# Performance work log

Hardware: AMD Instinct MI355X
Metric: run time of the kernel (lower is better)

Reference implementation:

```python
import jax, jax.numpy as jnp
import numpy as np

LEAKY = 0.2  # tf.nn.leaky_relu default alpha
E_SZ = [64, 64, 16]
F_SZ = [128, 128, 8]
N_MAPS, C, H, W = 64, 1, 32, 32
B = 8192


def _leaky(x):
    return jnp.where(x >= 0, x, LEAKY * x)


def func_theta(x, theta, sz, in_sz):
    # x: [B, in_sz]; theta: [B, total]; per-sample MLP with weights sliced from theta
    y = x
    offset = 0
    n = len(sz)
    for i, out_sz in enumerate(sz):
        w_sz = in_sz * out_sz
        Wm = theta[:, offset:offset + w_sz].reshape(-1, in_sz, out_sz)
        offset += w_sz
        b = theta[:, offset:offset + out_sz]
        offset += out_sz
        y = jnp.einsum('bi,bio->bo', y, Wm) + b
        if i < n - 1:
            y = _leaky(y)
        in_sz = out_sz
    return y


def setup_inputs() -> dict:
    key = jax.random.key(0)
    ks = jax.random.split(key, 16)

    def g(k, shape, scale):
        return (jax.random.normal(k, shape, dtype=jnp.float32) * scale)

    inp = {
        'indices': jax.random.randint(ks[0], (B,), 0, N_MAPS, dtype=jnp.int32),
        'states': jax.random.normal(ks[1], (B, 4), dtype=jnp.float32),
        'maps': jax.random.normal(ks[2], (N_MAPS, C, H, W), dtype=jnp.float32),
        'fc1_w': g(ks[3], (C * H * W, 256), 1.0 / np.sqrt(C * H * W)),
        'fc1_b': jnp.zeros((256,), jnp.float32),
        'fc2_w': g(ks[4], (256, 128), 1.0 / np.sqrt(256)),
        'fc2_b': jnp.zeros((128,), jnp.float32),
        'fc3_w': g(ks[5], (128, 128), 1.0 / np.sqrt(128)),
        'fc3_b': jnp.zeros((128,), jnp.float32),
        'bn_w': g(ks[6], (128, 32), 1.0 / np.sqrt(128)),
        'bn_b': jnp.zeros((32,), jnp.float32),
        'e_w': g(ks[7], (32, 5456), 1e-5),
        'e_b': g(ks[8], (5456,), 1e-3),
        'f_w': g(ks[9], (32, 21768), 1e-5),
        'f_b': g(ks[10], (21768,), 1e-3),
    }
    return inp


def reference(indices, states, maps, fc1_w, fc1_b, fc2_w, fc2_b, fc3_w, fc3_b,
              bn_w, bn_b, e_w, e_b, f_w, f_b):
    # gather maps per sample and flatten (NCHW -> NHWC transpose is a no-op after flatten
    # mathematically, but keep the exact data layout of the original)
    m = jnp.transpose(maps[indices], (0, 2, 3, 1)).astype(jnp.float32)  # [B,H,W,C]
    z = m.reshape(m.shape[0], -1)

    # hypernet trunk
    z = _leaky(z @ fc1_w + fc1_b)
    z = _leaky(z @ fc2_w + fc2_b)
    z = _leaky(z @ fc3_w + fc3_b)
    z = z @ bn_w + bn_b  # bottleneck, no activation
    theta_e = z @ e_w + e_b  # [B, 5456]
    theta_f = z @ f_w + f_b  # [B, 21768]

    S = states[:, 0:2]
    G = states[:, 2:4]
    e_s = func_theta(S, theta_e, E_SZ, 2)
    e_g = func_theta(G, theta_e, E_SZ, 2)
    zf = jnp.concatenate([e_s, e_g], axis=-1)  # [B, 32]
    ang = func_theta(zf, theta_f, F_SZ, 2 * E_SZ[-1])  # [B, 8]
    pts = jnp.concatenate([jnp.sin(ang), jnp.cos(ang)], axis=-1)  # [B, 16]
    return pts
```

## Files before the change

### kernel.cpp

```cpp
#include <hip/hip_runtime.h>
#include <hip/hip_bf16.h>


#define LEAKY 0.2f
#define NCLS 64
#define B_TOT 8192
#define NSLICE 4


__device__ __forceinline__ float lrelu(float x) { return x >= 0.f ? x : LEAKY * x; }

__global__ __launch_bounds__(1024) void backbone_bucket_kernel(
    const float* __restrict__ maps,
    const float* __restrict__ fc1_w, const float* __restrict__ fc1_b,
    const float* __restrict__ fc2_w, const float* __restrict__ fc2_b,
    const float* __restrict__ fc3_w, const float* __restrict__ fc3_b,
    const float* __restrict__ bn_w,  const float* __restrict__ bn_b,
    float* __restrict__ z,
    const int* __restrict__ idx, int* __restrict__ counts,
    int* __restrict__ offsets, int* __restrict__ perm)
{
    __shared__ float m[1024];
    __shared__ float red[1024];
    __shared__ float h1[256];
    __shared__ float h2[128];
    __shared__ float h3[128];
    __shared__ int cnt[16][64];
    __shared__ int wcur[16][64];

    const int t = threadIdx.x;

    if (blockIdx.x == 64) {
        const int w = t >> 6;
        cnt[w][t & 63] = 0;
        __syncthreads();
        int my[8];
#pragma unroll
        for (int r = 0; r < 8; ++r) {
            my[r] = idx[r * 1024 + t];
            atomicAdd(&cnt[w][my[r]], 1);
        }
        __syncthreads();
        if (t < 64) {
            int run = 0;
#pragma unroll
            for (int w2 = 0; w2 < 16; ++w2) {
                const int v = cnt[w2][t];
                wcur[w2][t] = run;
                run += v;
            }
            counts[t] = run;
            int x = run;
            for (int d = 1; d < 64; d <<= 1) {
                const int y = __shfl_up(x, d, 64);
                if (t >= d) x += y;
            }
            const int basec = x - run;
            offsets[t] = basec;
#pragma unroll
            for (int w2 = 0; w2 < 16; ++w2) wcur[w2][t] += basec;
        }
        __syncthreads();
#pragma unroll
        for (int r = 0; r < 8; ++r) {
            const int p = atomicAdd(&wcur[w][my[r]], 1);
            perm[p] = r * 1024 + t;
        }
        return;
    }

    const int c = blockIdx.x;
    m[t] = maps[(size_t)c * 1024 + t];
    __syncthreads();

    {
        const int o = t & 255, ks = t >> 8;
        const float* wp = fc1_w + o;
        float acc = 0.f;
#pragma unroll 8
        for (int i = 0; i < 256; ++i) {
            const int k = ks * 256 + i;
            acc += m[k] * wp[(size_t)k * 256];
        }
        red[t] = acc;
    }
    __syncthreads();
    if (t < 256)
        h1[t] = lrelu(fc1_b[t] + red[t] + red[256 + t] + red[512 + t] + red[768 + t]);
    __syncthreads();
    {
        const int o = t & 127, ks = t >> 7;
        float acc = 0.f;
#pragma unroll
        for (int i = 0; i < 32; ++i) {
            const int k = ks * 32 + i;
            acc += h1[k] * fc2_w[k * 128 + o];
        }
        red[t] = acc;
    }
    __syncthreads();
    if (t < 128) {
        float a = fc2_b[t];
#pragma unroll
        for (int r = 0; r < 8; ++r) a += red[r * 128 + t];
        h2[t] = lrelu(a);
    }
    __syncthreads();
    {
        const int o = t & 127, ks = t >> 7;
        float acc = 0.f;
#pragma unroll
        for (int i = 0; i < 16; ++i) {
            const int k = ks * 16 + i;
            acc += h2[k] * fc3_w[k * 128 + o];
        }
        red[t] = acc;
    }
    __syncthreads();
    if (t < 128) {
        float a = fc3_b[t];
#pragma unroll
        for (int r = 0; r < 8; ++r) a += red[r * 128 + t];
        h3[t] = lrelu(a);
    }
    __syncthreads();
    {
        const int o = t & 31, ks = t >> 5;
        float acc = 0.f;
#pragma unroll
        for (int i = 0; i < 4; ++i) {
            const int k = ks * 4 + i;
            acc += h3[k] * bn_w[k * 32 + o];
        }
        red[t] = acc;
    }
    __syncthreads();
    if (t < 32) {
        float a = bn_b[t];
#pragma unroll
        for (int r = 0; r < 32; ++r) a += red[r * 32 + t];
        z[c * 32 + t] = a;
    }
}

__global__ __launch_bounds__(256) void theta_kernel(
    const float* __restrict__ z,
    const float* __restrict__ e_w, const float* __restrict__ e_b,
    const float* __restrict__ f_w, const float* __restrict__ f_b,
    float* __restrict__ th_e, float* __restrict__ th_f)
{
    __shared__ __align__(16) float zl[2048];
    const int t = threadIdx.x;
    ((float4*)zl)[t]       = ((const float4*)z)[t];
    ((float4*)zl)[t + 256] = ((const float4*)z)[t + 256];
    __syncthreads();

    int j = blockIdx.x * 256 + t;
    const int cbase = blockIdx.y * 8;
    const float* wbase;
    float* op;
    int stride;
    float bias;
    if (j < 5456) {
        wbase = e_w + j; bias = e_b[j]; op = th_e + j; stride = 5456;
    } else {
        const int jj = j - 5456;
        if (jj >= 21768) return;
        wbase = f_w + jj; bias = f_b[jj]; op = th_f + jj; stride = 21768;
    }
    float wk[32];
#pragma unroll
    for (int k = 0; k < 32; ++k) wk[k] = wbase[(size_t)k * stride];

#pragma unroll
    for (int cc = 0; cc < 8; cc += 4) {
        const int c0 = cbase + cc;
        float a0 = bias, a1 = bias, a2 = bias, a3 = bias;
#pragma unroll
        for (int k4 = 0; k4 < 8; ++k4) {
            const float4 z0 = *(const float4*)&zl[(c0 + 0) * 32 + k4 * 4];
            const float4 z1 = *(const float4*)&zl[(c0 + 1) * 32 + k4 * 4];
            const float4 z2 = *(const float4*)&zl[(c0 + 2) * 32 + k4 * 4];
            const float4 z3 = *(const float4*)&zl[(c0 + 3) * 32 + k4 * 4];
            const float w0 = wk[k4 * 4], w1 = wk[k4 * 4 + 1];
            const float w2 = wk[k4 * 4 + 2], w3 = wk[k4 * 4 + 3];
            a0 += z0.x * w0 + z0.y * w1 + z0.z * w2 + z0.w * w3;
            a1 += z1.x * w0 + z1.y * w1 + z1.z * w2 + z1.w * w3;
            a2 += z2.x * w0 + z2.y * w1 + z2.z * w2 + z2.w * w3;
            a3 += z3.x * w0 + z3.y * w1 + z3.z * w2 + z3.w * w3;
        }
        op[(size_t)(c0 + 0) * stride] = a0;
        op[(size_t)(c0 + 1) * stride] = a1;
        op[(size_t)(c0 + 2) * stride] = a2;
        op[(size_t)(c0 + 3) * stride] = a3;
    }
}

#define ESTRIDE 68
#define FSTRIDE 132

__global__ __launch_bounds__(512) void func_kernel(
    const float* __restrict__ states,
    const float* __restrict__ th_e_all, const float* __restrict__ th_f_all,
    const int* __restrict__ counts, const int* __restrict__ offsets,
    const int* __restrict__ perm, float* __restrict__ out)
{
    __shared__ __align__(16) float wbuf[5392];
    __shared__ __align__(16) float w3fb[1160];
    __shared__ __align__(16) float actA[4352];
    __shared__ __align__(16) float actB[4352];

    const int c = blockIdx.x;
    const int s = blockIdx.y;
    const int nb   = counts[c];
    const int base = offsets[c];
    const int chunk = (nb + NSLICE - 1) / NSLICE;
    const int k0 = s * chunk;
    const int k1 = (nb < k0 + chunk) ? nb : (k0 + chunk);
    const int cnt = (k1 > k0) ? (k1 - k0) : 0;
    if (cnt == 0) return;

    const float* te = th_e_all + (size_t)c * 5456;
    const float* tf = th_f_all + (size_t)c * 21768;

    const int t  = threadIdx.x;
    const int b  = t & 31;
    const int ve = (t >> 5) & 1;
    const int vb = t & 63;
    const int ge = t >> 6;
    const int gf = t >> 5;
    const int cole = ge * 8;
    const int colf = gf * 8;
    const int eoff = vb * ESTRIDE;
    const int foff = b * FSTRIDE;

    for (int j = t * 4; j < 1160; j += 2048)
        *(float4*)&w3fb[j] = *(const float4*)&tf[20608 + j];
    for (int j = t * 4; j < 5392; j += 2048)
        *(float4*)&wbuf[j] = *(const float4*)&te[j];

    const int passes = (cnt + 31) >> 5;
    for (int p = 0; p < passes; ++p) {
        __syncthreads();
        if (p) {
            for (int j = t * 4; j < 5392; j += 2048)
                *(float4*)&wbuf[j] = *(const float4*)&te[j];
            __syncthreads();
        }

        const int kk = k0 + p * 32 + b;
        const bool valid = kk < k1;
        const int bi = valid ? perm[base + kk] : 0;
        const float2 sv = *(const float2*)&states[(size_t)bi * 4 + 2 * ve];

        {
            const float4 wa0 = *(const float4*)&wbuf[cole];
            const float4 wa1 = *(const float4*)&wbuf[cole + 4];
            const float4 wb0 = *(const float4*)&wbuf[64 + cole];
            const float4 wb1 = *(const float4*)&wbuf[64 + cole + 4];
            const float4 bb0 = *(const float4*)&wbuf[128 + cole];
            const float4 bb1 = *(const float4*)&wbuf[128 + cole + 4];
            float4 o0, o1;
            o0.x = lrelu(sv.x * wa0.x + sv.y * wb0.x + bb0.x);
            o0.y = lrelu(sv.x * wa0.y + sv.y * wb0.y + bb0.y);
            o0.z = lrelu(sv.x * wa0.z + sv.y * wb0.z + bb0.z);
            o0.w = lrelu(sv.x * wa0.w + sv.y * wb0.w + bb0.w);
            o1.x = lrelu(sv.x * wa1.x + sv.y * wb1.x + bb1.x);
            o1.y = lrelu(sv.x * wa1.y + sv.y * wb1.y + bb1.y);
            o1.z = lrelu(sv.x * wa1.z + sv.y * wb1.z + bb1.z);
            o1.w = lrelu(sv.x * wa1.w + sv.y * wb1.w + bb1.w);
            *(float4*)&actA[eoff + cole]     = o0;
            *(float4*)&actA[eoff + cole + 4] = o1;
        }
        __syncthreads();

        {
            float acc[8] = {0, 0, 0, 0, 0, 0, 0, 0};
#pragma unroll 4
            for (int i4 = 0; i4 < 16; ++i4) {
                const float4 y4 = *(const float4*)&actA[eoff + i4 * 4];
#pragma unroll
                for (int u = 0; u < 4; ++u) {
                    const int row = 192 + (i4 * 4 + u) * 64 + cole;
                    const float4 wA = *(const float4*)&wbuf[row];
                    const float4 wB = *(const float4*)&wbuf[row + 4];
                    const float yv = (&y4.x)[u];
                    acc[0] += yv * wA.x; acc[1] += yv * wA.y;
                    acc[2] += yv * wA.z; acc[3] += yv * wA.w;
                    acc[4] += yv * wB.x; acc[5] += yv * wB.y;
                    acc[6] += yv * wB.z; acc[7] += yv * wB.w;
                }
            }
            const float4 bA = *(const float4*)&wbuf[4288 + cole];
            const float4 bB = *(const float4*)&wbuf[4288 + cole + 4];
            float4 o0, o1;
            o0.x = lrelu(acc[0] + bA.x); o0.y = lrelu(acc[1] + bA.y);
            o0.z = lrelu(acc[2] + bA.z); o0.w = lrelu(acc[3] + bA.w);
            o1.x = lrelu(acc[4] + bB.x); o1.y = lrelu(acc[5] + bB.y);
            o1.z = lrelu(acc[6] + bB.z); o1.w = lrelu(acc[7] + bB.w);
            *(float4*)&actB[eoff + cole]     = o0;
            *(float4*)&actB[eoff + cole + 4] = o1;
        }
        __syncthreads();

        {
            const int col3 = ge * 2;
            float a0 = 0.f, a1 = 0.f;
#pragma unroll 4
            for (int i4 = 0; i4 < 16; ++i4) {
                const float4 y4 = *(const float4*)&actB[eoff + i4 * 4];
#pragma unroll
                for (int u = 0; u < 4; ++u) {
                    const int i = i4 * 4 + u;
                    const float yv = (&y4.x)[u];
                    a0 += yv * wbuf[4352 + i * 16 + col3];
                    a1 += yv * wbuf[4352 + i * 16 + col3 + 1];
                }
            }
            a0 += wbuf[5376 + col3];
            a1 += wbuf[5376 + col3 + 1];
            actA[foff + ve * 16 + col3]     = a0;
            actA[foff + ve * 16 + col3 + 1] = a1;
        }
        __syncthreads();

        for (int j = t * 4; j < 4224; j += 2048)
            *(float4*)&wbuf[j] = *(const float4*)&tf[j];
        __syncthreads();

        {
            float acc[8] = {0, 0, 0, 0, 0, 0, 0, 0};
#pragma unroll
            for (int i4 = 0; i4 < 8; ++i4) {
                const float4 y4 = *(const float4*)&actA[foff + i4 * 4];
#pragma unroll
                for (int u = 0; u < 4; ++u) {
                    const int row = (i4 * 4 + u) * 128 + colf;
                    const float4 wA = *(const float4*)&wbuf[row];
                    const float4 wB = *(const float4*)&wbuf[row + 4];
                    const float yv = (&y4.x)[u];
                    acc[0] += yv * wA.x; acc[1] += yv * wA.y;
                    acc[2] += yv * wA.z; acc[3] += yv * wA.w;
                    acc[4] += yv * wB.x; acc[5] += yv * wB.y;
                    acc[6] += yv * wB.z; acc[7] += yv * wB.w;
                }
            }
            const float4 bA = *(const float4*)&wbuf[4096 + colf];
            const float4 bB = *(const float4*)&wbuf[4096 + colf + 4];
            float4 o0, o1;
            o0.x = lrelu(acc[0] + bA.x); o0.y = lrelu(acc[1] + bA.y);
            o0.z = lrelu(acc[2] + bA.z); o0.w = lrelu(acc[3] + bA.w);
            o1.x = lrelu(acc[4] + bB.x); o1.y = lrelu(acc[5] + bB.y);
            o1.z = lrelu(acc[6] + bB.z); o1.w = lrelu(acc[7] + bB.w);
            *(float4*)&actB[foff + colf]     = o0;
            *(float4*)&actB[foff + colf + 4] = o1;
        }
        __syncthreads();

        {
            float acc[8] = {0, 0, 0, 0, 0, 0, 0, 0};
#pragma unroll
            for (int h = 0; h < 4; ++h) {
                if (h) __syncthreads();
                for (int j = t * 4; j < 4096; j += 2048)
                    *(float4*)&wbuf[j] = *(const float4*)&tf[4224 + h * 4096 + j];
                __syncthreads();
#pragma unroll 4
                for (int i4 = 0; i4 < 8; ++i4) {
                    const float4 y4 = *(const float4*)&actB[foff + h * 32 + i4 * 4];
#pragma unroll
                    for (int u = 0; u < 4; ++u) {
                        const int row = (i4 * 4 + u) * 128 + colf;
                        const float4 wA = *(const float4*)&wbuf[row];
                        const float4 wB = *(const float4*)&wbuf[row + 4];
                        const float yv = (&y4.x)[u];
                        acc[0] += yv * wA.x; acc[1] += yv * wA.y;
                        acc[2] += yv * wA.z; acc[3] += yv * wA.w;
                        acc[4] += yv * wB.x; acc[5] += yv * wB.y;
                        acc[6] += yv * wB.z; acc[7] += yv * wB.w;
                    }
                }
            }
            const float4 bA = *(const float4*)&w3fb[colf];
            const float4 bB = *(const float4*)&w3fb[colf + 4];
            float4 o0, o1;
            o0.x = lrelu(acc[0] + bA.x); o0.y = lrelu(acc[1] + bA.y);
            o0.z = lrelu(acc[2] + bA.z); o0.w = lrelu(acc[3] + bA.w);
            o1.x = lrelu(acc[4] + bB.x); o1.y = lrelu(acc[5] + bB.y);
            o1.z = lrelu(acc[6] + bB.z); o1.w = lrelu(acc[7] + bB.w);
            *(float4*)&actA[foff + colf]     = o0;
            *(float4*)&actA[foff + colf + 4] = o1;
        }
        __syncthreads();

        if (gf < 8) {
            float a = 0.f;
#pragma unroll 8
            for (int i4 = 0; i4 < 32; ++i4) {
                const float4 y4 = *(const float4*)&actA[foff + i4 * 4];
#pragma unroll
                for (int u = 0; u < 4; ++u)
                    a += (&y4.x)[u] * w3fb[128 + (i4 * 4 + u) * 8 + gf];
            }
            a += w3fb[1152 + gf];
            if (valid) {
                out[(size_t)bi * 16 + gf]     = __sinf(a);
                out[(size_t)bi * 16 + 8 + gf] = __cosf(a);
            }
        }
    }
}

extern "C" void kernel_launch(void* const* d_in, const int* in_sizes, int n_in,
                              void* d_out, int out_size, void* d_ws, size_t ws_size,
                              hipStream_t stream)
{
    const int*   indices = (const int*)  d_in[0];
    const float* states  = (const float*)d_in[1];
    const float* maps    = (const float*)d_in[2];
    const float* fc1_w   = (const float*)d_in[3];
    const float* fc1_b   = (const float*)d_in[4];
    const float* fc2_w   = (const float*)d_in[5];
    const float* fc2_b   = (const float*)d_in[6];
    const float* fc3_w   = (const float*)d_in[7];
    const float* fc3_b   = (const float*)d_in[8];
    const float* bn_w    = (const float*)d_in[9];
    const float* bn_b    = (const float*)d_in[10];
    const float* e_w     = (const float*)d_in[11];
    const float* e_b     = (const float*)d_in[12];
    const float* f_w     = (const float*)d_in[13];
    const float* f_b     = (const float*)d_in[14];
    float* out = (float*)d_out;

    float* ws   = (float*)d_ws;
    float* z    = ws;
    float* th_e = ws + 2048;
    float* th_f = ws + 351232;
    int* counts  = (int*)(ws + 1744384);
    int* offsets = counts + 64;
    int* perm    = counts + 128;

    backbone_bucket_kernel<<<65, 1024, 0, stream>>>(
        maps, fc1_w, fc1_b, fc2_w, fc2_b, fc3_w, fc3_b, bn_w, bn_b, z,
        indices, counts, offsets, perm);
    theta_kernel<<<dim3(107, 8), 256, 0, stream>>>(
        z, e_w, e_b, f_w, f_b, th_e, th_f);
    func_kernel<<<dim3(NCLS, NSLICE), 512, 0, stream>>>(
        states, th_e, th_f, counts, offsets, perm, out);
}
```

Baseline: 141.6 us.

## Register-tile per-sample MLP layers over multiple samples and vectorize backbone matvecs

The backbone kernel now computes four output columns per thread with float4 weight loads, uses more k-splits, and reduces the partial sums in float4. In the per-class function kernel, each thread now computes two output columns for four samples instead of eight columns for one sample, so each weight value read from shared memory is reused across four samples. The final 8-output layer is spread across all 512 threads by splitting the k range in two and reducing through a small shared buffer. The aim is to cut shared-memory weight traffic and idle lanes, in exchange for more register pressure and an extra sync and partial-sum buffer.

```diff
diff --git a/kernel.cpp b/kernel.cpp
--- a/kernel.cpp
+++ b/kernel.cpp
@@ -6,6 +6,8 @@
 #define NCLS 64
 #define B_TOT 8192
 #define NSLICE 4
+#define ESTRIDE 68
+#define FSTRIDE 132
 
 
 __device__ __forceinline__ float lrelu(float x) { return x >= 0.f ? x : LEAKY * x; }
@@ -21,10 +23,10 @@
     int* __restrict__ offsets, int* __restrict__ perm)
 {
     __shared__ float m[1024];
-    __shared__ float red[1024];
-    __shared__ float h1[256];
-    __shared__ float h2[128];
-    __shared__ float h3[128];
+    __shared__ __align__(16) float4 red4[1024];
+    __shared__ __align__(16) float h1[256];
+    __shared__ __align__(16) float h2[128];
+    __shared__ __align__(16) float h3[128];
     __shared__ int cnt[16][64];
     __shared__ int wcur[16][64];
 
@@ -74,72 +76,98 @@
     __syncthreads();
 
     {
-        const int o = t & 255, ks = t >> 8;
-        const float* wp = fc1_w + o;
-        float acc = 0.f;
+        const int og = t & 63, ks = t >> 6;
+        const float* wp = fc1_w + og * 4;
+        float4 acc = {0.f, 0.f, 0.f, 0.f};
 #pragma unroll 8
-        for (int i = 0; i < 256; ++i) {
-            const int k = ks * 256 + i;
-            acc += m[k] * wp[(size_t)k * 256];
-        }
-        red[t] = acc;
-    }
-    __syncthreads();
-    if (t < 256)
-        h1[t] = lrelu(fc1_b[t] + red[t] + red[256 + t] + red[512 + t] + red[768 + t]);
+        for (int i = 0; i < 64; ++i) {
+            const int k = ks * 64 + i;
+            const float mk = m[k];
+            const float4 w = *(const float4*)&wp[(size_t)k * 256];
+            acc.x += mk * w.x; acc.y += mk * w.y;
+            acc.z += mk * w.z; acc.w += mk * w.w;
+        }
+        red4[t] = acc;
+    }
+    __syncthreads();
+    if (t < 64) {
+        float4 a = *(const float4*)&fc1_b[t * 4];
+#pragma unroll
+        for (int r = 0; r < 16; ++r) {
+            const float4 v = red4[r * 64 + t];
+            a.x += v.x; a.y += v.y; a.z += v.z; a.w += v.w;
+        }
+        a.x = lrelu(a.x); a.y = lrelu(a.y); a.z = lrelu(a.z); a.w = lrelu(a.w);
+        *(float4*)&h1[t * 4] = a;
+    }
     __syncthreads();
     {
-        const int o = t & 127, ks = t >> 7;
-        float acc = 0.f;
-#pragma unroll
-        for (int i = 0; i < 32; ++i) {
-            const int k = ks * 32 + i;
-            acc += h1[k] * fc2_w[k * 128 + o];
-        }
-        red[t] = acc;
-    }
-    __syncthreads();
-    if (t < 128) {
-        float a = fc2_b[t];
-#pragma unroll
-        for (int r = 0; r < 8; ++r) a += red[r * 128 + t];
-        h2[t] = lrelu(a);
+        const int og = t & 31, ks = t >> 5;
+        float4 acc = {0.f, 0.f, 0.f, 0.f};
+#pragma unroll
+        for (int i = 0; i < 8; ++i) {
+            const int k = ks * 8 + i;
+            const float hk = h1[k];
+            const float4 w = *(const float4*)&fc2_w[k * 128 + og * 4];
+            acc.x += hk * w.x; acc.y += hk * w.y;
+            acc.z += hk * w.z; acc.w += hk * w.w;
+        }
+        red4[t] = acc;
+    }
+    __syncthreads();
+    if (t < 32) {
+        float4 a = *(const float4*)&fc2_b[t * 4];
+#pragma unroll
+        for (int r = 0; r < 32; ++r) {
+            const float4 v = red4[r * 32 + t];
+            a.x += v.x; a.y += v.y; a.z += v.z; a.w += v.w;
+        }
+        a.x = lrelu(a.x); a.y = lrelu(a.y); a.z = lrelu(a.z); a.w = lrelu(a.w);
+        *(float4*)&h2[t * 4] = a;
     }
     __syncthreads();
     {
-        const int o = t & 127, ks = t >> 7;
-        float acc = 0.f;
-#pragma unroll
-        for (int i = 0; i < 16; ++i) {
-            const int k = ks * 16 + i;
-            acc += h2[k] * fc3_w[k * 128 + o];
-        }
-        red[t] = acc;
-    }
-    __syncthreads();
-    if (t < 128) {
-        float a = fc3_b[t];
-#pragma unroll
-        for (int r = 0; r < 8; ++r) a += red[r * 128 + t];
-        h3[t] = lrelu(a);
-    }
-    __syncthreads();
-    {
-        const int o = t & 31, ks = t >> 5;
-        float acc = 0.f;
+        const int og = t & 31, ks = t >> 5;
+        float4 acc = {0.f, 0.f, 0.f, 0.f};
 #pragma unroll
         for (int i = 0; i < 4; ++i) {
             const int k = ks * 4 + i;
-            acc += h3[k] * bn_w[k * 32 + o];
-        }
-        red[t] = acc;
+            const float hk = h2[k];
+            const float4 w = *(const float4*)&fc3_w[k * 128 + og * 4];
+            acc.x += hk * w.x; acc.y += hk * w.y;
+            acc.z += hk * w.z; acc.w += hk * w.w;
+        }
+        red4[t] = acc;
     }
     __syncthreads();
     if (t < 32) {
-        float a = bn_b[t];
-#pragma unroll
-        for (int r = 0; r < 32; ++r) a += red[r * 32 + t];
-        z[c * 32 + t] = a;
+        float4 a = *(const float4*)&fc3_b[t * 4];
+#pragma unroll
+        for (int r = 0; r < 32; ++r) {
+            const float4 v = red4[r * 32 + t];
+            a.x += v.x; a.y += v.y; a.z += v.z; a.w += v.w;
+        }
+        a.x = lrelu(a.x); a.y = lrelu(a.y); a.z = lrelu(a.z); a.w = lrelu(a.w);
+        *(float4*)&h3[t * 4] = a;
+    }
+    __syncthreads();
+    {
+        const int og = t & 7, ks = t >> 3;
+        const float hk = h3[ks];
+        const float4 w = *(const float4*)&bn_w[ks * 32 + og * 4];
+        float4 acc;
+        acc.x = hk * w.x; acc.y = hk * w.y; acc.z = hk * w.z; acc.w = hk * w.w;
+        red4[t] = acc;
+    }
+    __syncthreads();
+    if (t < 8) {
+        float4 a = *(const float4*)&bn_b[t * 4];
+#pragma unroll
+        for (int r = 0; r < 128; ++r) {
+            const float4 v = red4[r * 8 + t];
+            a.x += v.x; a.y += v.y; a.z += v.z; a.w += v.w;
+        }
+        *(float4*)&z[c * 32 + t * 4] = a;
     }
 }
 
@@ -196,9 +224,6 @@
     }
 }
 
-#define ESTRIDE 68
-#define FSTRIDE 132
-
 __global__ __launch_bounds__(512) void func_kernel(
     const float* __restrict__ states,
     const float* __restrict__ th_e_all, const float* __restrict__ th_f_all,
@@ -209,6 +234,7 @@
     __shared__ __align__(16) float w3fb[1160];
     __shared__ __align__(16) float actA[4352];
     __shared__ __align__(16) float actB[4352];
+    __shared__ __align__(16) float part[512];
 
     const int c = blockIdx.x;
     const int s = blockIdx.y;
@@ -223,16 +249,11 @@
     const float* te = th_e_all + (size_t)c * 5456;
     const float* tf = th_f_all + (size_t)c * 21768;
 
-    const int t  = threadIdx.x;
-    const int b  = t & 31;
-    const int ve = (t >> 5) & 1;
-    const int vb = t & 63;
-    const int ge = t >> 6;
-    const int gf = t >> 5;
-    const int cole = ge * 8;
-    const int colf = gf * 8;
-    const int eoff = vb * ESTRIDE;
-    const int foff = b * FSTRIDE;
+    const int t   = threadIdx.x;
+    const int vbs = t & 15;
+    const int ce  = (t >> 4) * 2;
+    const int fbs = t & 7;
+    const int cf  = (t >> 3) * 2;
 
     for (int j = t * 4; j < 1160; j += 2048)
         *(float4*)&w3fb[j] = *(const float4*)&tf[20608 + j];
@@ -248,79 +269,81 @@
             __syncthreads();
         }
 
-        const int kk = k0 + p * 32 + b;
-        const bool valid = kk < k1;
-        const int bi = valid ? perm[base + kk] : 0;
-        const float2 sv = *(const float2*)&states[(size_t)bi * 4 + 2 * ve];
+        const int kkA = k0 + p * 32 + vbs;
+        const int kkB = kkA + 16;
+        const int biA = (kkA < k1) ? perm[base + kkA] : 0;
+        const int biB = (kkB < k1) ? perm[base + kkB] : 0;
+        const float4 stA = *(const float4*)&states[(size_t)biA * 4];
+        const float4 stB = *(const float4*)&states[(size_t)biB * 4];
+        const float i0[4] = {stA.x, stB.x, stA.z, stB.z};
+        const float i1[4] = {stA.y, stB.y, stA.w, stB.w};
 
         {
-            const float4 wa0 = *(const float4*)&wbuf[cole];
-            const float4 wa1 = *(const float4*)&wbuf[cole + 4];
-            const float4 wb0 = *(const float4*)&wbuf[64 + cole];
-            const float4 wb1 = *(const float4*)&wbuf[64 + cole + 4];
-            const float4 bb0 = *(const float4*)&wbuf[128 + cole];
-            const float4 bb1 = *(const float4*)&wbuf[128 + cole + 4];
-            float4 o0, o1;
-            o0.x = lrelu(sv.x * wa0.x + sv.y * wb0.x + bb0.x);
-            o0.y = lrelu(sv.x * wa0.y + sv.y * wb0.y + bb0.y);
-            o0.z = lrelu(sv.x * wa0.z + sv.y * wb0.z + bb0.z);
-            o0.w = lrelu(sv.x * wa0.w + sv.y * wb0.w + bb0.w);
-            o1.x = lrelu(sv.x * wa1.x + sv.y * wb1.x + bb1.x);
-            o1.y = lrelu(sv.x * wa1.y + sv.y * wb1.y + bb1.y);
-            o1.z = lrelu(sv.x * wa1.z + sv.y * wb1.z + bb1.z);
-            o1.w = lrelu(sv.x * wa1.w + sv.y * wb1.w + bb1.w);
-            *(float4*)&actA[eoff + cole]     = o0;
-            *(float4*)&actA[eoff + cole + 4] = o1;
+            const float2 wa = *(const float2*)&wbuf[ce];
+            const float2 wb = *(const float2*)&wbuf[64 + ce];
+            const float2 bb = *(const float2*)&wbuf[128 + ce];
+#pragma unroll
+            for (int j = 0; j < 4; ++j) {
+                float2 o;
+                o.x = lrelu(i0[j] * wa.x + i1[j] * wb.x + bb.x);
+                o.y = lrelu(i0[j] * wa.y + i1[j] * wb.y + bb.y);
+                *(float2*)&actA[(vbs + 16 * j) * ESTRIDE + ce] = o;
+            }
         }
         __syncthreads();
 
         {
-            float acc[8] = {0, 0, 0, 0, 0, 0, 0, 0};
+            float a0[4] = {0, 0, 0, 0}, a1[4] = {0, 0, 0, 0};
 #pragma unroll 4
-            for (int i4 = 0; i4 < 16; ++i4) {
-                const float4 y4 = *(const float4*)&actA[eoff + i4 * 4];
+            for (int k4 = 0; k4 < 16; ++k4) {
+                float4 y[4];
+#pragma unroll
+                for (int j = 0; j < 4; ++j)
+                    y[j] = *(const float4*)&actA[(vbs + 16 * j) * ESTRIDE + k4 * 4];
 #pragma unroll
                 for (int u = 0; u < 4; ++u) {
-                    const int row = 192 + (i4 * 4 + u) * 64 + cole;
-                    const float4 wA = *(const float4*)&wbuf[row];
-                    const float4 wB = *(const float4*)&wbuf[row + 4];
-                    const float yv = (&y4.x)[u];
-                    acc[0] += yv * wA.x; acc[1] += yv * wA.y;
-                    acc[2] += yv * wA.z; acc[3] += yv * wA.w;
-                    acc[4] += yv * wB.x; acc[5] += yv * wB.y;
-                    acc[6] += yv * wB.z; acc[7] += yv * wB.w;
+                    const float2 w = *(const float2*)&wbuf[192 + (k4 * 4 + u) * 64 + ce];
+#pragma unroll
+                    for (int j = 0; j < 4; ++j) {
+                        const float yv = (&y[j].x)[u];
+                        a0[j] += yv * w.x;
+                        a1[j] += yv * w.y;
+                    }
                 }
             }
-            const float4 bA = *(const float4*)&wbuf[4288 + cole];
-            const float4 bB = *(const float4*)&wbuf[4288 + cole + 4];
-            float4 o0, o1;
-            o0.x = lrelu(acc[0] + bA.x); o0.y = lrelu(acc[1] + bA.y);
-            o0.z = lrelu(acc[2] + bA.z); o0.w = lrelu(acc[3] + bA.w);
-            o1.x = lrelu(acc[4] + bB.x); o1.y = lrelu(acc[5] + bB.y);
-            o1.z = lrelu(acc[6] + bB.z); o1.w = lrelu(acc[7] + bB.w);
-            *(float4*)&actB[eoff + cole]     = o0;
-            *(float4*)&actB[eoff + cole + 4] = o1;
-        }
-        __syncthreads();
-
-        {
-            const int col3 = ge * 2;
-            float a0 = 0.f, a1 = 0.f;
+            const float2 b2 = *(const float2*)&wbuf[4288 + ce];
+#pragma unroll
+            for (int j = 0; j < 4; ++j) {
+                float2 o;
+                o.x = lrelu(a0[j] + b2.x);
+                o.y = lrelu(a1[j] + b2.y);
+                *(float2*)&actB[(vbs + 16 * j) * ESTRIDE + ce] = o;
+            }
+        }
+        __syncthreads();
+
+        if (t < 256) {
+            const int c3 = t >> 4;
+            float a[4] = {0, 0, 0, 0};
 #pragma unroll 4
-            for (int i4 = 0; i4 < 16; ++i4) {
-                const float4 y4 = *(const float4*)&actB[eoff + i4 * 4];
+            for (int k4 = 0; k4 < 16; ++k4) {
+                float4 y[4];
+#pragma unroll
+                for (int j = 0; j < 4; ++j)
+                    y[j] = *(const float4*)&actB[(vbs + 16 * j) * ESTRIDE + k4 * 4];
 #pragma unroll
                 for (int u = 0; u < 4; ++u) {
-                    const int i = i4 * 4 + u;
-                    const float yv = (&y4.x)[u];
-                    a0 += yv * wbuf[4352 + i * 16 + col3];
-                    a1 += yv * wbuf[4352 + i * 16 + col3 + 1];
+                    const float w = wbuf[4352 + (k4 * 4 + u) * 16 + c3];
+#pragma unroll
+                    for (int j = 0; j < 4; ++j) a[j] += (&y[j].x)[u] * w;
                 }
             }
-            a0 += wbuf[5376 + col3];
-            a1 += wbuf[5376 + col3 + 1];
-            actA[foff + ve * 16 + col3]     = a0;
-            actA[foff + ve * 16 + col3 + 1] = a1;
+            const float b3 = wbuf[5376 + c3];
+#pragma unroll
+            for (int j = 0; j < 4; ++j) {
+                const int vb = vbs + 16 * j;
+                actA[(vb & 31) * FSTRIDE + (vb >> 5) * 16 + c3] = a[j] + b3;
+            }
         }
         __syncthreads();
 
@@ -329,36 +352,37 @@
         __syncthreads();
 
         {
-            float acc[8] = {0, 0, 0, 0, 0, 0, 0, 0};
-#pragma unroll
-            for (int i4 = 0; i4 < 8; ++i4) {
-                const float4 y4 = *(const float4*)&actA[foff + i4 * 4];
+            float a0[4] = {0, 0, 0, 0}, a1[4] = {0, 0, 0, 0};
+#pragma unroll
+            for (int k4 = 0; k4 < 8; ++k4) {
+                float4 y[4];
+#pragma unroll
+                for (int j = 0; j < 4; ++j)
+                    y[j] = *(const float4*)&actA[(fbs + 8 * j) * FSTRIDE + k4 * 4];
 #pragma unroll
                 for (int u = 0; u < 4; ++u) {
-                    const int row = (i4 * 4 + u) * 128 + colf;
-                    const float4 wA = *(const float4*)&wbuf[row];
-                    const float4 wB = *(const float4*)&wbuf[row + 4];
-                    const float yv = (&y4.x)[u];
-                    acc[0] += yv * wA.x; acc[1] += yv * wA.y;
-                    acc[2] += yv * wA.z; acc[3] += yv * wA.w;
-                    acc[4] += yv * wB.x; acc[5] += yv * wB.y;
-                    acc[6] += yv * wB.z; acc[7] += yv * wB.w;
+                    const float2 w = *(const float2*)&wbuf[(k4 * 4 + u) * 128 + cf];
+#pragma unroll
+                    for (int j = 0; j < 4; ++j) {
+                        const float yv = (&y[j].x)[u];
+                        a0[j] += yv * w.x;
+                        a1[j] += yv * w.y;
+                    }
                 }
             }
-            const float4 bA = *(const float4*)&wbuf[4096 + colf];
-            const float4 bB = *(const float4*)&wbuf[4096 + colf + 4];
-            float4 o0, o1;
-            o0.x = lrelu(acc[0] + bA.x); o0.y = lrelu(acc[1] + bA.y);
-            o0.z = lrelu(acc[2] + bA.z); o0.w = lrelu(acc[3] + bA.w);
-            o1.x = lrelu(acc[4] + bB.x); o1.y = lrelu(acc[5] + bB.y);
-            o1.z = lrelu(acc[6] + bB.z); o1.w = lrelu(acc[7] + bB.w);
-            *(float4*)&actB[foff + colf]     = o0;
-            *(float4*)&actB[foff + colf + 4] = o1;
+            const float2 b1 = *(const float2*)&wbuf[4096 + cf];
+#pragma unroll
+            for (int j = 0; j < 4; ++j) {
+                float2 o;
+                o.x = lrelu(a0[j] + b1.x);
+                o.y = lrelu(a1[j] + b1.y);
+                *(float2*)&actB[(fbs + 8 * j) * FSTRIDE + cf] = o;
+            }
         }
         __syncthreads();
 
         {
-            float acc[8] = {0, 0, 0, 0, 0, 0, 0, 0};
+            float a0[4] = {0, 0, 0, 0}, a1[4] = {0, 0, 0, 0};
 #pragma unroll
             for (int h = 0; h < 4; ++h) {
                 if (h) __syncthreads();
@@ -366,46 +390,56 @@
                     *(float4*)&wbuf[j] = *(const float4*)&tf[4224 + h * 4096 + j];
                 __syncthreads();
 #pragma unroll 4
-                for (int i4 = 0; i4 < 8; ++i4) {
-                    const float4 y4 = *(const float4*)&actB[foff + h * 32 + i4 * 4];
+                for (int k4 = 0; k4 < 8; ++k4) {
+                    float4 y[4];
+#pragma unroll
+                    for (int j = 0; j < 4; ++j)
+                        y[j] = *(const float4*)&actB[(fbs + 8 * j) * FSTRIDE + h * 32 + k4 * 4];
 #pragma unroll
                     for (int u = 0; u < 4; ++u) {
-                        const int row = (i4 * 4 + u) * 128 + colf;
-                        const float4 wA = *(const float4*)&wbuf[row];
-                        const float4 wB = *(const float4*)&wbuf[row + 4];
-                        const float yv = (&y4.x)[u];
-                        acc[0] += yv * wA.x; acc[1] += yv * wA.y;
-                        acc[2] += yv * wA.z; acc[3] += yv * wA.w;
-                        acc[4] += yv * wB.x; acc[5] += yv * wB.y;
-                        acc[6] += yv * wB.z; acc[7] += yv * wB.w;
+                        const float2 w = *(const float2*)&wbuf[(k4 * 4 + u) * 128 + cf];
+#pragma unroll
+                        for (int j = 0; j < 4; ++j) {
+                            const float yv = (&y[j].x)[u];
+                            a0[j] += yv * w.x;
+                            a1[j] += yv * w.y;
+                        }
                     }
                 }
             }
-            const float4 bA = *(const float4*)&w3fb[colf];
-            const float4 bB = *(const float4*)&w3fb[colf + 4];
-            float4 o0, o1;
-            o0.x = lrelu(acc[0] + bA.x); o0.y = lrelu(acc[1] + bA.y);
-            o0.z = lrelu(acc[2] + bA.z); o0.w = lrelu(acc[3] + bA.w);
-            o1.x = lrelu(acc[4] + bB.x); o1.y = lrelu(acc[5] + bB.y);
-            o1.z = lrelu(acc[6] + bB.z); o1.w = lrelu(acc[7] + bB.w);
-            *(float4*)&actA[foff + colf]     = o0;
-            *(float4*)&actA[foff + colf + 4] = o1;
-        }
-        __syncthreads();
-
-        if (gf < 8) {
+            const float2 b2 = *(const float2*)&w3fb[cf];
+#pragma unroll
+            for (int j = 0; j < 4; ++j) {
+                float2 o;
+                o.x = lrelu(a0[j] + b2.x);
+                o.y = lrelu(a1[j] + b2.y);
+                *(float2*)&actA[(fbs + 8 * j) * FSTRIDE + cf] = o;
+            }
+        }
+        __syncthreads();
+
+        {
+            const int bat = t & 31, c8 = (t >> 5) & 7, kh = t >> 8;
             float a = 0.f;
-#pragma unroll 8
-            for (int i4 = 0; i4 < 32; ++i4) {
-                const float4 y4 = *(const float4*)&actA[foff + i4 * 4];
+#pragma unroll 4
+            for (int k4 = kh * 16; k4 < kh * 16 + 16; ++k4) {
+                const float4 y = *(const float4*)&actA[bat * FSTRIDE + k4 * 4];
 #pragma unroll
                 for (int u = 0; u < 4; ++u)
-                    a += (&y4.x)[u] * w3fb[128 + (i4 * 4 + u) * 8 + gf];
-            }
-            a += w3fb[1152 + gf];
-            if (valid) {
-                out[(size_t)bi * 16 + gf]     = __sinf(a);
-                out[(size_t)bi * 16 + 8 + gf] = __cosf(a);
+                    a += (&y.x)[u] * w3fb[128 + (k4 * 4 + u) * 8 + c8];
+            }
+            part[kh * 256 + bat * 8 + c8] = a;
+        }
+        __syncthreads();
+        if (t < 256) {
+            const int bat = t & 31, c8 = t >> 5;
+            const int kk = k0 + p * 32 + bat;
+            if (kk < k1) {
+                const int bi = perm[base + kk];
+                const float a = part[bat * 8 + c8] + part[256 + bat * 8 + c8]
+                              + w3fb[1152 + c8];
+                out[(size_t)bi * 16 + c8]     = __sinf(a);
+                out[(size_t)bi * 16 + 8 + c8] = __cosf(a);
             }
         }
     }
```

New measurement: 146.4 us. 1.03x slower.
